# Kernel tuning notes

Measured on AMD Instinct MI355X. Metric: run time of the kernel, lower is better.

The kernel has to match this reference:

```python
import math
import jax, jax.numpy as jnp
import numpy as np

NUM_LAYERS = 4
D_MODEL = 1024
N_HEAD = 8
HEAD_DIM = D_MODEL // N_HEAD
B, L = 8, 512
EPS = 1e-5


def setup_inputs() -> dict:
    key = jax.random.key(0)
    ks = jax.random.split(key, 6)
    x = jax.random.normal(ks[0], (B, L, D_MODEL), dtype=jnp.float32)
    mask = jnp.ones((B, L), dtype=jnp.int32)
    qv_w = jax.random.normal(ks[1], (NUM_LAYERS, 2 * D_MODEL, D_MODEL), dtype=jnp.float32) * 0.02
    r_r_bias = jax.random.normal(ks[2], (NUM_LAYERS, N_HEAD, HEAD_DIM), dtype=jnp.float32) * 0.02
    r_w_bias = jax.random.normal(ks[3], (NUM_LAYERS, N_HEAD, HEAD_DIM), dtype=jnp.float32) * 0.02
    ffn_w = jax.random.normal(ks[4], (NUM_LAYERS, D_MODEL, D_MODEL), dtype=jnp.float32) * 0.02
    ffn_b = jnp.zeros((NUM_LAYERS, D_MODEL), dtype=jnp.float32)
    ln1_g = jnp.ones((NUM_LAYERS, D_MODEL), dtype=jnp.float32)
    ln1_b = jnp.zeros((NUM_LAYERS, D_MODEL), dtype=jnp.float32)
    ln2_g = jnp.ones((NUM_LAYERS, D_MODEL), dtype=jnp.float32)
    ln2_b = jnp.zeros((NUM_LAYERS, D_MODEL), dtype=jnp.float32)
    return dict(x=x, mask=mask, qv_w=qv_w, r_r_bias=r_r_bias, r_w_bias=r_w_bias,
                ln1_g=ln1_g, ln1_b=ln1_b, ffn_w=ffn_w, ffn_b=ffn_b,
                ln2_g=ln2_g, ln2_b=ln2_b)


def _rel_pos_embed(seq_len, dim):
    # weights[p + origin_shift] encodes sinusoid of relative position p;
    # selected positions are arange(-seq_len, seq_len) -> shape [2L, dim]
    half = dim // 2
    inv_freq = jnp.exp(jnp.arange(half, dtype=jnp.float32) * (-math.log(10000.0) / (half - 1)))
    pos = jnp.arange(-seq_len, seq_len, dtype=jnp.float32)
    ang = pos[:, None] * inv_freq[None, :]
    return jnp.concatenate([jnp.sin(ang), jnp.cos(ang)], axis=1)  # [2L, dim]


def _shift(BD):
    # [b,n,L,2L] -> [b,n,L,L] Transformer-XL shift trick
    b, n, l, _ = BD.shape
    BD = jnp.concatenate([BD, jnp.zeros((b, n, l, 1), BD.dtype)], axis=-1)
    BD = BD.reshape(b, n, -1, l)[:, :, :-1].reshape(b, n, l, -1)
    return BD[:, :, :, l:]


def _layernorm(x, g, b):
    mu = jnp.mean(x, axis=-1, keepdims=True)
    var = jnp.mean(jnp.square(x - mu), axis=-1, keepdims=True)
    return (x - mu) * jax.lax.rsqrt(var + EPS) * g + b


def _rel_attn(x, mask, qv_w, rr, rw, pe):
    b, l, d = x.shape
    qv = x @ qv_w.T                      # [b,l,2d]
    q, v = jnp.split(qv, 2, axis=-1)
    q = q.reshape(b, l, N_HEAD, HEAD_DIM).transpose(0, 2, 1, 3)
    k = x.reshape(b, l, N_HEAD, HEAD_DIM).transpose(0, 2, 1, 3)  # raw x as keys (per source)
    v = v.reshape(b, l, N_HEAD, HEAD_DIM).transpose(0, 2, 1, 3)
    AC = jnp.einsum('bnqd,bnkd->bnqk', q + rr[:, None], k)
    D_ = jnp.einsum('nd,ld->nl', rw, pe)[None, :, None]          # [1,n,1,2L]
    B_ = jnp.einsum('bnqd,ld->bnql', q, pe)                      # [b,n,L,2L]
    BD = _shift(B_ + D_)
    attn = AC + BD                                               # scale = 1
    attn = jnp.where(mask[:, None, None, :] == 0, -jnp.inf, attn)
    attn = jax.nn.softmax(attn, axis=-1)
    out = jnp.einsum('bnqk,bnkd->bqnd', attn, v).reshape(b, l, d)
    return out


def reference(x, mask, qv_w, r_r_bias, r_w_bias, ln1_g, ln1_b, ffn_w, ffn_b, ln2_g, ln2_b):
    pe = _rel_pos_embed(x.shape[1], HEAD_DIM)
    h = x
    for i in range(NUM_LAYERS):
        res = h
        h = _rel_attn(h, mask, qv_w[i], r_r_bias[i], r_w_bias[i], pe)
        h = _layernorm(h + res, ln1_g[i], ln1_b[i])
        res = h
        h = jax.nn.relu(h @ ffn_w[i].T + ffn_b[i])
        h = _layernorm(res + h, ln2_g[i], ln2_b[i])
    return h
```

## Files before the change

### kernel.cpp

```cpp
#include <hip/hip_runtime.h>
#include <math.h>

#define NL 4
#define DM 1024
#define NH 8
#define HD 128
#define BB 8
#define LL 512
#define MM (BB*LL)
#define PEN (2*LL)
#define QT 64
#define KT 32
#define NKT (LL/KT)
#define VS 44

typedef __attribute__((ext_vector_type(8))) __bf16 bf16x8;
typedef __attribute__((ext_vector_type(4))) float f32x4;

__device__ __forceinline__ unsigned short f2b(float f) {
  unsigned int u = __float_as_uint(f);
  u = (u + 0x7FFFu + ((u >> 16) & 1u)) >> 16;
  return (unsigned short)u;
}
__device__ __forceinline__ float b2f(unsigned short s) {
  return __uint_as_float(((unsigned int)s) << 16);
}
__device__ __forceinline__ void glds16(const void* g, void* l) {
  __builtin_amdgcn_global_load_lds(
      (const __attribute__((address_space(1))) unsigned int*)g,
      (__attribute__((address_space(3))) unsigned int*)l, 16, 0, 0);
}
union U8 { unsigned short s[8]; bf16x8 v; };
__device__ __forceinline__ void split8(const float4& a, const float4& b,
                                       bf16x8& h, bf16x8& l) {
  float x[8] = {a.x,a.y,a.z,a.w,b.x,b.y,b.z,b.w};
  U8 uh, ul;
#pragma unroll
  for (int e = 0; e < 8; ++e) {
    unsigned u = __float_as_uint(x[e]);
    uh.s[e] = (unsigned short)(u >> 16);
    ul.s[e] = f2b(x[e] - __uint_as_float(u & 0xffff0000u));
  }
  h = uh.v; l = ul.v;
}

__global__ __launch_bounds__(256) void pe_kernel(unsigned short* __restrict__ peh,
                                                 unsigned short* __restrict__ pel) {
  int idx = blockIdx.x * 256 + threadIdx.x;
  if (idx >= PEN * HD) return;
  int p = idx / HD, j = idx % HD;
  int tt = (j < 64) ? j : (j - 64);
  float invf = expf((float)tt * (-9.210340371976184f / 63.0f));
  float ang = (float)(p - LL) * invf;
  float v = (j < 64) ? sinf(ang) : cosf(ang);
  unsigned short h = f2b(v);
  peh[idx] = h;
  pel[idx] = f2b(v - b2f(h));
}

__global__ __launch_bounds__(256) void d2_kernel(const float* __restrict__ rrb,
                                                 const float* __restrict__ rwb,
                                                 const unsigned short* __restrict__ peh,
                                                 const unsigned short* __restrict__ pel,
                                                 float* __restrict__ d2) {
  int idx = blockIdx.x * 256 + threadIdx.x;
  if (idx >= NH * PEN) return;
  int n = idx / PEN, p = idx % PEN;
  float s = 0.f;
  for (int d = 0; d < HD; ++d) {
    float pv = b2f(peh[p*HD + d]) + b2f(pel[p*HD + d]);
    s += (rwb[n*HD + d] - rrb[n*HD + d]) * pv;
  }
  d2[idx] = s;
}

__global__ __launch_bounds__(256) void split_kernel(const float* __restrict__ in,
                                                    unsigned short* __restrict__ hi,
                                                    unsigned short* __restrict__ lo,
                                                    int n) {
  int i = (blockIdx.x * 256 + threadIdx.x) * 4;
  if (i >= n) return;
  float4 v = *(const float4*)&in[i];
  float x[4] = {v.x, v.y, v.z, v.w};
  ushort4 h4, l4;
  unsigned short* hp = (unsigned short*)&h4;
  unsigned short* lp = (unsigned short*)&l4;
#pragma unroll
  for (int e = 0; e < 4; ++e) {
    unsigned short h = f2b(x[e]);
    hp[e] = h;
    lp[e] = f2b(x[e] - b2f(h));
  }
  *(ushort4*)&hi[i] = h4;
  *(ushort4*)&lo[i] = l4;
}

template<bool FFN>
__global__ __launch_bounds__(256) void gemm_mfma(
    const unsigned short* __restrict__ Ah, const unsigned short* __restrict__ Al,
    const float* __restrict__ Bw, const float* __restrict__ bias,
    float* __restrict__ C, unsigned short* __restrict__ Vhi,
    unsigned short* __restrict__ Vlo, int N, int K, int ldc) {
  __shared__ __align__(16) unsigned short AsH[128*64];
  __shared__ __align__(16) unsigned short AsL[128*64];
  __shared__ __align__(16) unsigned short BsH[128*72];
  __shared__ __align__(16) unsigned short BsL[128*72];
  const int t = threadIdx.x;
  const int w = t >> 6, l = t & 63;
  const int gx = gridDim.x;
  const int nwg = gx * gridDim.y;
  const int id = blockIdx.y * gx + blockIdx.x;
  const int swz = (id & 7) * (nwg >> 3) + (id >> 3);
  const int bm = (swz / gx) * 128, bn = (swz % gx) * 128;
  const int wr = (w >> 1) * 64, wc = (w & 1) * 64;

  const int aseg = ((t & 7) ^ ((t >> 3) & 7)) * 8;
  const unsigned short* Ahb = Ah + (size_t)(bm + (t >> 3)) * K + aseg;
  const unsigned short* Alb = Al + (size_t)(bm + (t >> 3)) * K + aseg;

  const int brow = t >> 1, bhalf = (t & 1) * 32;
  const float* Bb = Bw + (size_t)(bn + brow) * K + bhalf;

  f32x4 acc[4][4] = {};
  const int lm = l & 15;
  const int lg = l >> 4;

  for (int k0 = 0; k0 < K; k0 += 64) {
    float4 bv[8];
#pragma unroll
    for (int c = 0; c < 8; ++c)
      bv[c] = *(const float4*)(Bb + k0 + c*4);
#pragma unroll
    for (int i = 0; i < 4; ++i) {
      glds16(Ahb + (size_t)(i*32)*K + k0, &AsH[w*512 + i*2048]);
      glds16(Alb + (size_t)(i*32)*K + k0, &AsL[w*512 + i*2048]);
    }
#pragma unroll
    for (int c = 0; c < 8; ++c) {
      float xs[4] = {bv[c].x, bv[c].y, bv[c].z, bv[c].w};
      ushort4 h4, l4;
      unsigned short* hp = (unsigned short*)&h4;
      unsigned short* lp = (unsigned short*)&l4;
#pragma unroll
      for (int e = 0; e < 4; ++e) {
        unsigned u = __float_as_uint(xs[e]);
        hp[e] = (unsigned short)(u >> 16);
        float r = xs[e] - __uint_as_float(u & 0xffff0000u);
        lp[e] = (unsigned short)(__float_as_uint(r) >> 16);
      }
      *(ushort4*)&BsH[brow*72 + bhalf + c*4] = h4;
      *(ushort4*)&BsL[brow*72 + bhalf + c*4] = l4;
    }
    __syncthreads();

#pragma unroll
    for (int kk = 0; kk < 2; ++kk) {
      bf16x8 afh[4], afl[4], bfh[4], bfl[4];
#pragma unroll
      for (int i = 0; i < 4; ++i) {
        const int row = wr + i*16 + lm;
        const int sw = ((kk*4 + lg) ^ (lm & 7)) * 8;
        afh[i] = *(const bf16x8*)&AsH[row*64 + sw];
        afl[i] = *(const bf16x8*)&AsL[row*64 + sw];
      }
#pragma unroll
      for (int j = 0; j < 4; ++j) {
        bfh[j] = *(const bf16x8*)&BsH[(wc + j*16 + lm)*72 + kk*32 + lg*8];
        bfl[j] = *(const bf16x8*)&BsL[(wc + j*16 + lm)*72 + kk*32 + lg*8];
      }
#pragma unroll
      for (int i = 0; i < 4; ++i)
#pragma unroll
        for (int j = 0; j < 4; ++j) {
          acc[i][j] = __builtin_amdgcn_mfma_f32_16x16x32_bf16(afh[i], bfh[j], acc[i][j], 0, 0, 0);
          acc[i][j] = __builtin_amdgcn_mfma_f32_16x16x32_bf16(afh[i], bfl[j], acc[i][j], 0, 0, 0);
          acc[i][j] = __builtin_amdgcn_mfma_f32_16x16x32_bf16(afl[i], bfh[j], acc[i][j], 0, 0, 0);
        }
    }
    __syncthreads();
  }

  const int cr = (l >> 4) * 4;
  const bool vhalf = (!FFN) && (bn >= DM);
#pragma unroll
  for (int i = 0; i < 4; ++i) {
#pragma unroll
    for (int j = 0; j < 4; ++j) {
      int row = bm + wr + i*16 + cr;
      int col = bn + wc + j*16 + lm;
      float bvl = FFN ? bias[col] : 0.f;
      f32x4 a = acc[i][j];
#pragma unroll
      for (int r4 = 0; r4 < 4; ++r4) {
        float v = a[r4];
        if (FFN) {
          v = fmaxf(v + bvl, 0.f);
          C[(size_t)(row + r4) * ldc + col] = v;
        } else if (vhalf) {
          unsigned u = __float_as_uint(v);
          size_t off = (size_t)(row + r4) * DM + (col - DM);
          Vhi[off] = (unsigned short)(u >> 16);
          Vlo[off] = f2b(v - __uint_as_float(u & 0xffff0000u));
        } else {
          C[(size_t)(row + r4) * ldc + col] = v;
        }
      }
    }
  }
}

__global__ __launch_bounds__(256, 2) void attn_mfma(
    const float* __restrict__ qbuf,
    const unsigned short* __restrict__ khp,
    const unsigned short* __restrict__ klp,
    const unsigned short* __restrict__ vhp,
    const unsigned short* __restrict__ vlp,
    const unsigned short* __restrict__ pehp,
    const unsigned short* __restrict__ pelp,
    const float* __restrict__ rrb,
    const int*   __restrict__ mask,
    const float* __restrict__ d2p,
    float* __restrict__ outp)
{
  __shared__ __align__(16) unsigned short KsH[KT*136];
  __shared__ __align__(16) unsigned short KsL[KT*136];
  __shared__ __align__(16) unsigned short VtH[HD*VS];
  __shared__ __align__(16) unsigned short VtL[HD*VS];
  __shared__ __align__(16) unsigned short PsH[4][16*40];
  __shared__ __align__(16) unsigned short PsL[4][16*40];

  const int id = blockIdx.x + 8*blockIdx.y + 64*blockIdx.z;
  const int n  = id & 7;
  const int qt = (id >> 3) & 7;
  const int b  = id >> 6;
  const int q0 = qt * QT;
  const int t  = threadIdx.x;
  const int w  = t >> 6, l = t & 63;
  const int lm = l & 15, lg = l >> 4;
  const int q0w = q0 + w*16;
  const int r8 = t >> 3, s8 = t & 7;
  const int vr0 = t >> 5, vd4 = (t & 31)*4;

  bf16x8 qah[4], qal[4];
  {
    size_t qrow = (size_t)(b*LL + q0w + lm) * DM + (size_t)n*HD;
#pragma unroll
    for (int c = 0; c < 4; ++c) {
      int d0 = c*32 + lg*8;
      float4 x1 = *(const float4*)&qbuf[qrow + d0];
      float4 x2 = *(const float4*)&qbuf[qrow + d0 + 4];
      float4 r1 = *(const float4*)&rrb[n*HD + d0];
      float4 r2 = *(const float4*)&rrb[n*HD + d0 + 4];
      float4 a = {x1.x+r1.x, x1.y+r1.y, x1.z+r1.z, x1.w+r1.w};
      float4 bq = {x2.x+r2.x, x2.y+r2.y, x2.z+r2.z, x2.w+r2.w};
      split8(a, bq, qah[c], qal[c]);
    }
  }

  {
    size_t krow = (size_t)(b*LL + r8)*DM + (size_t)n*HD + s8*16;
    *(uint4*)&KsH[r8*136 + s8*16]     = *(const uint4*)&khp[krow];
    *(uint4*)&KsH[r8*136 + s8*16 + 8] = *(const uint4*)&khp[krow + 8];
    *(uint4*)&KsL[r8*136 + s8*16]     = *(const uint4*)&klp[krow];
    *(uint4*)&KsL[r8*136 + s8*16 + 8] = *(const uint4*)&klp[krow + 8];
    ushort4 vh[4], vl[4];
#pragma unroll
    for (int i = 0; i < 4; ++i) {
      size_t vrow = (size_t)(b*LL + vr0*4 + i)*DM + n*HD + vd4;
      vh[i] = *(const ushort4*)&vhp[vrow];
      vl[i] = *(const ushort4*)&vlp[vrow];
    }
#pragma unroll
    for (int e = 0; e < 4; ++e) {
      ushort4 th = { ((const unsigned short*)&vh[0])[e], ((const unsigned short*)&vh[1])[e],
                     ((const unsigned short*)&vh[2])[e], ((const unsigned short*)&vh[3])[e] };
      ushort4 tl = { ((const unsigned short*)&vl[0])[e], ((const unsigned short*)&vl[1])[e],
                     ((const unsigned short*)&vl[2])[e], ((const unsigned short*)&vl[3])[e] };
      *(ushort4*)&VtH[(vd4+e)*VS + vr0*4] = th;
      *(ushort4*)&VtL[(vd4+e)*VS + vr0*4] = tl;
    }
  }
  __syncthreads();

  float m_run[4] = {-3.0e38f, -3.0e38f, -3.0e38f, -3.0e38f};
  float l_run[4] = {0.f, 0.f, 0.f, 0.f};
  f32x4 accO[8] = {};
  f32x4 accB0 = {}, accB1 = {}, accB2 = {};

  for (int kt = 0; kt < NKT; ++kt) {
    const int k0 = kt * KT;
    const int base_w = k0 - q0w + 497;

    uint4 kxh0, kxh1, kxl0, kxl1;
    ushort4 vxh[4], vxl[4];
    const bool pf = kt < NKT-1;
    if (pf) {
      size_t krow = (size_t)(b*LL + k0 + KT + r8)*DM + (size_t)n*HD + s8*16;
      kxh0 = *(const uint4*)&khp[krow];     kxh1 = *(const uint4*)&khp[krow + 8];
      kxl0 = *(const uint4*)&klp[krow];     kxl1 = *(const uint4*)&klp[krow + 8];
#pragma unroll
      for (int i = 0; i < 4; ++i) {
        size_t vrow = (size_t)(b*LL + k0 + KT + vr0*4 + i)*DM + n*HD + vd4;
        vxh[i] = *(const ushort4*)&vhp[vrow];
        vxl[i] = *(const ushort4*)&vlp[vrow];
      }
    }

    float d2v1, d2v2;
    {
      int di1 = base_w + 16 + lm; di1 = di1 > PEN-1 ? PEN-1 : di1;
      int di2 = base_w + 32 + lm; di2 = di2 > PEN-1 ? PEN-1 : di2;
      d2v1 = d2p[n*PEN + di1];
      d2v2 = d2p[n*PEN + di2];
    }
    const int msk0 = mask[b*LL + k0 + lm];
    const int msk1 = mask[b*LL + k0 + 16 + lm];

    bf16x8 p1h[4], p1l[4], p2h[4], p2l[4];
    {
      int pr1 = base_w + 16 + lm; pr1 = pr1 > PEN-1 ? PEN-1 : pr1;
      int pr2 = base_w + 32 + lm; pr2 = pr2 > PEN-1 ? PEN-1 : pr2;
      const unsigned short* pb1 = pehp + (size_t)pr1*HD + lg*8;
      const unsigned short* pq1 = pelp + (size_t)pr1*HD + lg*8;
      const unsigned short* pb2 = pehp + (size_t)pr2*HD + lg*8;
      const unsigned short* pq2 = pelp + (size_t)pr2*HD + lg*8;
#pragma unroll
      for (int c = 0; c < 4; ++c) {
        p1h[c] = *(const bf16x8*)(pb1 + c*32);
        p1l[c] = *(const bf16x8*)(pq1 + c*32);
        p2h[c] = *(const bf16x8*)(pb2 + c*32);
        p2l[c] = *(const bf16x8*)(pq2 + c*32);
      }
    }

    __builtin_amdgcn_s_setprio(1);
    f32x4 accA[2] = {};
#pragma unroll
    for (int tt = 0; tt < 2; ++tt)
#pragma unroll
      for (int c = 0; c < 4; ++c) {
        const int krow = tt*16 + lm;
        bf16x8 kfh = *(const bf16x8*)&KsH[krow*136 + (c*4+lg)*8];
        bf16x8 kfl = *(const bf16x8*)&KsL[krow*136 + (c*4+lg)*8];
        accA[tt] = __builtin_amdgcn_mfma_f32_16x16x32_bf16(qah[c], kfh, accA[tt], 0, 0, 0);
        accA[tt] = __builtin_amdgcn_mfma_f32_16x16x32_bf16(qah[c], kfl, accA[tt], 0, 0, 0);
        accA[tt] = __builtin_amdgcn_mfma_f32_16x16x32_bf16(qal[c], kfh, accA[tt], 0, 0, 0);
      }

    if (kt == 0) {
      int pr0 = base_w + lm; pr0 = pr0 > PEN-1 ? PEN-1 : pr0;
      const unsigned short* pb0 = pehp + (size_t)pr0*HD + lg*8;
      const unsigned short* pq0 = pelp + (size_t)pr0*HD + lg*8;
      f32x4 a = {};
#pragma unroll
      for (int c = 0; c < 4; ++c) {
        bf16x8 ph = *(const bf16x8*)(pb0 + c*32);
        bf16x8 pl = *(const bf16x8*)(pq0 + c*32);
        a = __builtin_amdgcn_mfma_f32_16x16x32_bf16(qah[c], ph, a, 0, 0, 0);
        a = __builtin_amdgcn_mfma_f32_16x16x32_bf16(qah[c], pl, a, 0, 0, 0);
        a = __builtin_amdgcn_mfma_f32_16x16x32_bf16(qal[c], ph, a, 0, 0, 0);
      }
      float dv0 = d2p[n*PEN + pr0];
#pragma unroll
      for (int r = 0; r < 4; ++r) a[r] += dv0;
      accB0 = a;
    } else {
      accB0 = accB2;
    }
    {
      f32x4 a = {};
#pragma unroll
      for (int c = 0; c < 4; ++c) {
        a = __builtin_amdgcn_mfma_f32_16x16x32_bf16(qah[c], p1h[c], a, 0, 0, 0);
        a = __builtin_amdgcn_mfma_f32_16x16x32_bf16(qah[c], p1l[c], a, 0, 0, 0);
        a = __builtin_amdgcn_mfma_f32_16x16x32_bf16(qal[c], p1h[c], a, 0, 0, 0);
      }
#pragma unroll
      for (int r = 0; r < 4; ++r) a[r] += d2v1;
      accB1 = a;
    }
    {
      f32x4 a = {};
#pragma unroll
      for (int c = 0; c < 4; ++c) {
        a = __builtin_amdgcn_mfma_f32_16x16x32_bf16(qah[c], p2h[c], a, 0, 0, 0);
        a = __builtin_amdgcn_mfma_f32_16x16x32_bf16(qah[c], p2l[c], a, 0, 0, 0);
        a = __builtin_amdgcn_mfma_f32_16x16x32_bf16(qal[c], p2h[c], a, 0, 0, 0);
      }
#pragma unroll
      for (int r = 0; r < 4; ++r) a[r] += d2v2;
      accB2 = a;
    }
    __builtin_amdgcn_s_setprio(0);

    float s[2][4];
#pragma unroll
    for (int r = 0; r < 4; ++r) {
      const int qi = lg*4 + r;
      const int jm = (lm - qi + 15) & 15;
      const int src = (l & 48) | jm;
      const bool carry = lm > qi;
      float sh0 = __shfl(accB0[r], src);
      float sh1 = __shfl(accB1[r], src);
      float sh2 = __shfl(accB2[r], src);
      float bd0 = carry ? sh1 : sh0;
      float bd1 = carry ? sh2 : sh1;
      float v0 = accA[0][r] + bd0;
      float v1 = accA[1][r] + bd1;
      s[0][r] = (msk0 == 0) ? -1e30f : v0;
      s[1][r] = (msk1 == 0) ? -1e30f : v1;
    }

    float mt4[4];
    int allold = 1;
#pragma unroll
    for (int r = 0; r < 4; ++r) {
      float mt = fmaxf(s[0][r], s[1][r]);
      mt = fmaxf(mt, __shfl_xor(mt, 1));
      mt = fmaxf(mt, __shfl_xor(mt, 2));
      mt = fmaxf(mt, __shfl_xor(mt, 4));
      mt = fmaxf(mt, __shfl_xor(mt, 8));
      mt4[r] = mt;
      allold &= (mt <= m_run[r]) ? 1 : 0;
    }
    if (!__all(allold)) {
#pragma unroll
      for (int r = 0; r < 4; ++r) {
        float mn = fmaxf(m_run[r], mt4[r]);
        float sc = __expf(m_run[r] - mn);
        m_run[r] = mn;
        l_run[r] *= sc;
#pragma unroll
        for (int j8 = 0; j8 < 8; ++j8) accO[j8][r] *= sc;
      }
    }
#pragma unroll
    for (int r = 0; r < 4; ++r) {
      float p0 = __expf(s[0][r] - m_run[r]);
      float p1 = __expf(s[1][r] - m_run[r]);
      s[0][r] = p0; s[1][r] = p1;
      float la = p0 + p1;
      la += __shfl_xor(la, 1);
      la += __shfl_xor(la, 2);
      la += __shfl_xor(la, 4);
      la += __shfl_xor(la, 8);
      l_run[r] += la;
    }

#pragma unroll
    for (int tt = 0; tt < 2; ++tt)
#pragma unroll
      for (int r = 0; r < 4; ++r) {
        int qi = lg*4 + r, kc = tt*16 + lm;
        float p = s[tt][r];
        unsigned u = __float_as_uint(p);
        PsH[w][qi*40 + kc] = (unsigned short)(u >> 16);
        PsL[w][qi*40 + kc] = f2b(p - __uint_as_float(u & 0xffff0000u));
      }

    {
      __builtin_amdgcn_s_setprio(1);
      bf16x8 pah = *(const bf16x8*)&PsH[w][lm*40 + lg*8];
      bf16x8 pal = *(const bf16x8*)&PsL[w][lm*40 + lg*8];
#pragma unroll
      for (int j8 = 0; j8 < 8; ++j8) {
        const int dim = j8*16 + lm;
        bf16x8 vfh = *(const bf16x8*)&VtH[dim*VS + lg*8];
        bf16x8 vfl = *(const bf16x8*)&VtL[dim*VS + lg*8];
        accO[j8] = __builtin_amdgcn_mfma_f32_16x16x32_bf16(pah, vfh, accO[j8], 0, 0, 0);
        accO[j8] = __builtin_amdgcn_mfma_f32_16x16x32_bf16(pah, vfl, accO[j8], 0, 0, 0);
        accO[j8] = __builtin_amdgcn_mfma_f32_16x16x32_bf16(pal, vfh, accO[j8], 0, 0, 0);
      }
      __builtin_amdgcn_s_setprio(0);
    }

    __syncthreads();

    if (pf) {
      *(uint4*)&KsH[r8*136 + s8*16]     = kxh0;
      *(uint4*)&KsH[r8*136 + s8*16 + 8] = kxh1;
      *(uint4*)&KsL[r8*136 + s8*16]     = kxl0;
      *(uint4*)&KsL[r8*136 + s8*16 + 8] = kxl1;
#pragma unroll
      for (int e = 0; e < 4; ++e) {
        ushort4 th = { ((const unsigned short*)&vxh[0])[e], ((const unsigned short*)&vxh[1])[e],
                       ((const unsigned short*)&vxh[2])[e], ((const unsigned short*)&vxh[3])[e] };
        ushort4 tl = { ((const unsigned short*)&vxl[0])[e], ((const unsigned short*)&vxl[1])[e],
                       ((const unsigned short*)&vxl[2])[e], ((const unsigned short*)&vxl[3])[e] };
        *(ushort4*)&VtH[(vd4+e)*VS + vr0*4] = th;
        *(ushort4*)&VtL[(vd4+e)*VS + vr0*4] = tl;
      }
    }
    __syncthreads();
  }

  float inv[4];
#pragma unroll
  for (int r = 0; r < 4; ++r) inv[r] = 1.0f / l_run[r];
#pragma unroll
  for (int j8 = 0; j8 < 8; ++j8)
#pragma unroll
    for (int r = 0; r < 4; ++r)
      outp[(size_t)(b*LL + q0w + lg*4 + r)*DM + n*HD + j8*16 + lm] = accO[j8][r] * inv[r];
}

__global__ __launch_bounds__(256) void add_ln_kernel(
    const float* __restrict__ y, int ys,
    const float* __restrict__ res,
    const float* __restrict__ g, const float* __restrict__ bt,
    float* __restrict__ out,
    unsigned short* __restrict__ ohi, unsigned short* __restrict__ olo)
{
  const int r = blockIdx.x, t = threadIdx.x;
  float4 v = *(const float4*)&y[(size_t)r*ys + t*4];
  float4 w = *(const float4*)&res[(size_t)r*DM + t*4];
  float4 s = {v.x+w.x, v.y+w.y, v.z+w.z, v.w+w.w};
  float sum = s.x + s.y + s.z + s.w;
  float ssq = s.x*s.x + s.y*s.y + s.z*s.z + s.w*s.w;
#pragma unroll
  for (int off = 32; off >= 1; off >>= 1) {
    sum += __shfl_down(sum, off);
    ssq += __shfl_down(ssq, off);
  }
  __shared__ float red[8];
  int wid = t >> 6;
  if ((t & 63) == 0) { red[wid] = sum; red[wid+4] = ssq; }
  __syncthreads();
  float totS = red[0] + red[1] + red[2] + red[3];
  float totQ = red[4] + red[5] + red[6] + red[7];
  float mu  = totS * (1.0f/DM);
  float var = totQ * (1.0f/DM) - mu*mu;
  float inv = rsqrtf(var + 1e-5f);
  float4 gg = *(const float4*)&g[t*4];
  float4 bb = *(const float4*)&bt[t*4];
  float4 o;
  o.x = (s.x - mu)*inv*gg.x + bb.x;
  o.y = (s.y - mu)*inv*gg.y + bb.y;
  o.z = (s.z - mu)*inv*gg.z + bb.z;
  o.w = (s.w - mu)*inv*gg.w + bb.w;
  *(float4*)&out[(size_t)r*DM + t*4] = o;
  float xs[4] = {o.x, o.y, o.z, o.w};
  ushort4 h4, l4;
  unsigned short* hp = (unsigned short*)&h4;
  unsigned short* lp = (unsigned short*)&l4;
#pragma unroll
  for (int e = 0; e < 4; ++e) {
    unsigned short h = f2b(xs[e]);
    hp[e] = h;
    lp[e] = f2b(xs[e] - b2f(h));
  }
  *(ushort4*)&ohi[(size_t)r*DM + t*4] = h4;
  *(ushort4*)&olo[(size_t)r*DM + t*4] = l4;
}

extern "C" void kernel_launch(void* const* d_in, const int* in_sizes, int n_in,
                              void* d_out, int out_size, void* d_ws, size_t ws_size,
                              hipStream_t stream) {
  const float* x    = (const float*)d_in[0];
  const int*   mask = (const int*)d_in[1];
  const float* qv_w = (const float*)d_in[2];
  const float* rrb  = (const float*)d_in[3];
  const float* rwb  = (const float*)d_in[4];
  const float* ln1g = (const float*)d_in[5];
  const float* ln1b = (const float*)d_in[6];
  const float* ffnw = (const float*)d_in[7];
  const float* ffnb = (const float*)d_in[8];
  const float* ln2g = (const float*)d_in[9];
  const float* ln2b = (const float*)d_in[10];

  float* h  = (float*)d_out;
  unsigned short* peh = (unsigned short*)d_ws;
  unsigned short* pel = peh + (size_t)PEN*HD;
  float* d2   = (float*)(pel + (size_t)PEN*HD);
  float* qbuf = d2 + (size_t)NH*PEN;
  unsigned short* vhi = (unsigned short*)(qbuf + (size_t)MM*DM);
  unsigned short* vlo = vhi + (size_t)MM*DM;
  unsigned short* hhi = vlo + (size_t)MM*DM;
  unsigned short* hlo = hhi + (size_t)MM*DM;

  hipMemcpyAsync(h, x, (size_t)MM*DM*sizeof(float), hipMemcpyDeviceToDevice, stream);
  split_kernel<<<(MM*DM)/1024, 256, 0, stream>>>(x, hhi, hlo, MM*DM);
  pe_kernel<<<(PEN*HD)/256, 256, 0, stream>>>(peh, pel);

  for (int l = 0; l < NL; ++l) {
    const float* rr_l = rrb + (size_t)l*NH*HD;
    const float* rw_l = rwb + (size_t)l*NH*HD;
    d2_kernel<<<(NH*PEN)/256, 256, 0, stream>>>(rr_l, rw_l, peh, pel, d2);
    gemm_mfma<false><<<dim3((2*DM)/128, MM/128), 256, 0, stream>>>(
        hhi, hlo, qv_w + (size_t)l*2*DM*DM, nullptr, qbuf, vhi, vlo, 2*DM, DM, DM);
    attn_mfma<<<dim3(LL/QT, NH, BB), 256, 0, stream>>>(
        qbuf, hhi, hlo, vhi, vlo, peh, pel, rr_l, mask, d2, qbuf);
    add_ln_kernel<<<MM, 256, 0, stream>>>(qbuf, DM, h,
        ln1g + (size_t)l*DM, ln1b + (size_t)l*DM, h, hhi, hlo);
    gemm_mfma<true><<<dim3(DM/128, MM/128), 256, 0, stream>>>(
        hhi, hlo, ffnw + (size_t)l*DM*DM, ffnb + (size_t)l*DM, qbuf, nullptr, nullptr, DM, DM, DM);
    add_ln_kernel<<<MM, 256, 0, stream>>>(qbuf, DM, h,
        ln2g + (size_t)l*DM, ln2b + (size_t)l*DM, h, hhi, hlo);
  }
  (void)in_sizes; (void)n_in; (void)out_size; (void)ws_size;
}
```

Measured before the change: 914.9 us.

## Halve attention query tile, drop K-low LDS staging, read K-low fragments from global

The attention kernel now uses 32-query tiles with 128 threads (2 waves) instead of 64 queries with 256 threads, doubling the grid and reordering block indices so heads vary fastest. The low-part bf16 K tile is no longer staged in shared memory. Each wave loads its K-low fragments straight from global and issues those MFMAs after the positional-term work. This cuts LDS footprint and per-block staging, but raises global traffic for K-low and V reloads per query tile. The kt==0 positional index is now also clamped at zero.

```diff
diff --git a/kernel.cpp b/kernel.cpp
--- a/kernel.cpp
+++ b/kernel.cpp
@@ -9,7 +9,7 @@
 #define LL 512
 #define MM (BB*LL)
 #define PEN (2*LL)
-#define QT 64
+#define QT 32
 #define KT 32
 #define NKT (LL/KT)
 #define VS 44
@@ -209,7 +209,7 @@
   }
 }
 
-__global__ __launch_bounds__(256, 2) void attn_mfma(
+__global__ __launch_bounds__(128, 2) void attn_mfma(
     const float* __restrict__ qbuf,
     const unsigned short* __restrict__ khp,
     const unsigned short* __restrict__ klp,
@@ -223,23 +223,21 @@
     float* __restrict__ outp)
 {
   __shared__ __align__(16) unsigned short KsH[KT*136];
-  __shared__ __align__(16) unsigned short KsL[KT*136];
   __shared__ __align__(16) unsigned short VtH[HD*VS];
   __shared__ __align__(16) unsigned short VtL[HD*VS];
-  __shared__ __align__(16) unsigned short PsH[4][16*40];
-  __shared__ __align__(16) unsigned short PsL[4][16*40];
-
-  const int id = blockIdx.x + 8*blockIdx.y + 64*blockIdx.z;
-  const int n  = id & 7;
-  const int qt = (id >> 3) & 7;
-  const int b  = id >> 6;
+  __shared__ __align__(16) unsigned short PsH[2][16*40];
+  __shared__ __align__(16) unsigned short PsL[2][16*40];
+
+  const int n  = blockIdx.x;
+  const int qt = blockIdx.y;
+  const int b  = blockIdx.z;
   const int q0 = qt * QT;
   const int t  = threadIdx.x;
   const int w  = t >> 6, l = t & 63;
   const int lm = l & 15, lg = l >> 4;
   const int q0w = q0 + w*16;
-  const int r8 = t >> 3, s8 = t & 7;
-  const int vr0 = t >> 5, vd4 = (t & 31)*4;
+  const int kr  = t >> 2, ks = (t & 3) * 32;
+  const int vr0 = (t >> 5) * 8, vd4 = (t & 31)*4;
 
   bf16x8 qah[4], qal[4];
   {
@@ -258,26 +256,31 @@
   }
 
   {
-    size_t krow = (size_t)(b*LL + r8)*DM + (size_t)n*HD + s8*16;
-    *(uint4*)&KsH[r8*136 + s8*16]     = *(const uint4*)&khp[krow];
-    *(uint4*)&KsH[r8*136 + s8*16 + 8] = *(const uint4*)&khp[krow + 8];
-    *(uint4*)&KsL[r8*136 + s8*16]     = *(const uint4*)&klp[krow];
-    *(uint4*)&KsL[r8*136 + s8*16 + 8] = *(const uint4*)&klp[krow + 8];
-    ushort4 vh[4], vl[4];
-#pragma unroll
-    for (int i = 0; i < 4; ++i) {
-      size_t vrow = (size_t)(b*LL + vr0*4 + i)*DM + n*HD + vd4;
+    size_t krow = (size_t)(b*LL + kr)*DM + (size_t)n*HD + ks;
+#pragma unroll
+    for (int i = 0; i < 4; ++i)
+      *(uint4*)&KsH[kr*136 + ks + i*8] = *(const uint4*)&khp[krow + i*8];
+    ushort4 vh[8], vl[8];
+#pragma unroll
+    for (int i = 0; i < 8; ++i) {
+      size_t vrow = (size_t)(b*LL + vr0 + i)*DM + n*HD + vd4;
       vh[i] = *(const ushort4*)&vhp[vrow];
       vl[i] = *(const ushort4*)&vlp[vrow];
     }
 #pragma unroll
     for (int e = 0; e < 4; ++e) {
-      ushort4 th = { ((const unsigned short*)&vh[0])[e], ((const unsigned short*)&vh[1])[e],
+      ushort4 ta = { ((const unsigned short*)&vh[0])[e], ((const unsigned short*)&vh[1])[e],
                      ((const unsigned short*)&vh[2])[e], ((const unsigned short*)&vh[3])[e] };
-      ushort4 tl = { ((const unsigned short*)&vl[0])[e], ((const unsigned short*)&vl[1])[e],
+      ushort4 tb = { ((const unsigned short*)&vh[4])[e], ((const unsigned short*)&vh[5])[e],
+                     ((const unsigned short*)&vh[6])[e], ((const unsigned short*)&vh[7])[e] };
+      ushort4 tc = { ((const unsigned short*)&vl[0])[e], ((const unsigned short*)&vl[1])[e],
                      ((const unsigned short*)&vl[2])[e], ((const unsigned short*)&vl[3])[e] };
-      *(ushort4*)&VtH[(vd4+e)*VS + vr0*4] = th;
-      *(ushort4*)&VtL[(vd4+e)*VS + vr0*4] = tl;
+      ushort4 td = { ((const unsigned short*)&vl[4])[e], ((const unsigned short*)&vl[5])[e],
+                     ((const unsigned short*)&vl[6])[e], ((const unsigned short*)&vl[7])[e] };
+      *(ushort4*)&VtH[(vd4+e)*VS + vr0]     = ta;
+      *(ushort4*)&VtH[(vd4+e)*VS + vr0 + 4] = tb;
+      *(ushort4*)&VtL[(vd4+e)*VS + vr0]     = tc;
+      *(ushort4*)&VtL[(vd4+e)*VS + vr0 + 4] = td;
     }
   }
   __syncthreads();
@@ -291,16 +294,17 @@
     const int k0 = kt * KT;
     const int base_w = k0 - q0w + 497;
 
-    uint4 kxh0, kxh1, kxl0, kxl1;
-    ushort4 vxh[4], vxl[4];
+    uint4 kxh[4];
+    ushort4 vxh[8], vxl[8];
     const bool pf = kt < NKT-1;
     if (pf) {
-      size_t krow = (size_t)(b*LL + k0 + KT + r8)*DM + (size_t)n*HD + s8*16;
-      kxh0 = *(const uint4*)&khp[krow];     kxh1 = *(const uint4*)&khp[krow + 8];
-      kxl0 = *(const uint4*)&klp[krow];     kxl1 = *(const uint4*)&klp[krow + 8];
-#pragma unroll
-      for (int i = 0; i < 4; ++i) {
-        size_t vrow = (size_t)(b*LL + k0 + KT + vr0*4 + i)*DM + n*HD + vd4;
+      size_t krow = (size_t)(b*LL + k0 + KT + kr)*DM + (size_t)n*HD + ks;
+#pragma unroll
+      for (int i = 0; i < 4; ++i)
+        kxh[i] = *(const uint4*)&khp[krow + i*8];
+#pragma unroll
+      for (int i = 0; i < 8; ++i) {
+        size_t vrow = (size_t)(b*LL + k0 + KT + vr0 + i)*DM + n*HD + vd4;
         vxh[i] = *(const ushort4*)&vhp[vrow];
         vxl[i] = *(const ushort4*)&vlp[vrow];
       }
@@ -315,6 +319,13 @@
     }
     const int msk0 = mask[b*LL + k0 + lm];
     const int msk1 = mask[b*LL + k0 + 16 + lm];
+
+    bf16x8 klo_f[2][4];
+#pragma unroll
+    for (int tt = 0; tt < 2; ++tt)
+#pragma unroll
+      for (int c = 0; c < 4; ++c)
+        klo_f[tt][c] = *(const bf16x8*)&klp[(size_t)(b*LL + k0 + tt*16 + lm)*DM + n*HD + c*32 + lg*8];
 
     bf16x8 p1h[4], p1l[4], p2h[4], p2l[4];
     {
@@ -339,16 +350,14 @@
     for (int tt = 0; tt < 2; ++tt)
 #pragma unroll
       for (int c = 0; c < 4; ++c) {
-        const int krow = tt*16 + lm;
-        bf16x8 kfh = *(const bf16x8*)&KsH[krow*136 + (c*4+lg)*8];
-        bf16x8 kfl = *(const bf16x8*)&KsL[krow*136 + (c*4+lg)*8];
+        const int krw = tt*16 + lm;
+        bf16x8 kfh = *(const bf16x8*)&KsH[krw*136 + (c*4+lg)*8];
         accA[tt] = __builtin_amdgcn_mfma_f32_16x16x32_bf16(qah[c], kfh, accA[tt], 0, 0, 0);
-        accA[tt] = __builtin_amdgcn_mfma_f32_16x16x32_bf16(qah[c], kfl, accA[tt], 0, 0, 0);
         accA[tt] = __builtin_amdgcn_mfma_f32_16x16x32_bf16(qal[c], kfh, accA[tt], 0, 0, 0);
       }
 
     if (kt == 0) {
-      int pr0 = base_w + lm; pr0 = pr0 > PEN-1 ? PEN-1 : pr0;
+      int pr0 = base_w + lm; pr0 = pr0 < 0 ? 0 : (pr0 > PEN-1 ? PEN-1 : pr0);
       const unsigned short* pb0 = pehp + (size_t)pr0*HD + lg*8;
       const unsigned short* pq0 = pelp + (size_t)pr0*HD + lg*8;
       f32x4 a = {};
@@ -391,6 +400,12 @@
       for (int r = 0; r < 4; ++r) a[r] += d2v2;
       accB2 = a;
     }
+
+#pragma unroll
+    for (int tt = 0; tt < 2; ++tt)
+#pragma unroll
+      for (int c = 0; c < 4; ++c)
+        accA[tt] = __builtin_amdgcn_mfma_f32_16x16x32_bf16(qah[c], klo_f[tt][c], accA[tt], 0, 0, 0);
     __builtin_amdgcn_s_setprio(0);
 
     float s[2][4];
@@ -477,18 +492,23 @@
     __syncthreads();
 
     if (pf) {
-      *(uint4*)&KsH[r8*136 + s8*16]     = kxh0;
-      *(uint4*)&KsH[r8*136 + s8*16 + 8] = kxh1;
-      *(uint4*)&KsL[r8*136 + s8*16]     = kxl0;
-      *(uint4*)&KsL[r8*136 + s8*16 + 8] = kxl1;
+#pragma unroll
+      for (int i = 0; i < 4; ++i)
+        *(uint4*)&KsH[kr*136 + ks + i*8] = kxh[i];
 #pragma unroll
       for (int e = 0; e < 4; ++e) {
-        ushort4 th = { ((const unsigned short*)&vxh[0])[e], ((const unsigned short*)&vxh[1])[e],
+        ushort4 ta = { ((const unsigned short*)&vxh[0])[e], ((const unsigned short*)&vxh[1])[e],
                        ((const unsigned short*)&vxh[2])[e], ((const unsigned short*)&vxh[3])[e] };
-        ushort4 tl = { ((const unsigned short*)&vxl[0])[e], ((const unsigned short*)&vxl[1])[e],
+        ushort4 tb = { ((const unsigned short*)&vxh[4])[e], ((const unsigned short*)&vxh[5])[e],
+                       ((const unsigned short*)&vxh[6])[e], ((const unsigned short*)&vxh[7])[e] };
+        ushort4 tc = { ((const unsigned short*)&vxl[0])[e], ((const unsigned short*)&vxl[1])[e],
                        ((const unsigned short*)&vxl[2])[e], ((const unsigned short*)&vxl[3])[e] };
-        *(ushort4*)&VtH[(vd4+e)*VS + vr0*4] = th;
-        *(ushort4*)&VtL[(vd4+e)*VS + vr0*4] = tl;
+        ushort4 td = { ((const unsigned short*)&vxl[4])[e], ((const unsigned short*)&vxl[5])[e],
+                       ((const unsigned short*)&vxl[6])[e], ((const unsigned short*)&vxl[7])[e] };
+        *(ushort4*)&VtH[(vd4+e)*VS + vr0]     = ta;
+        *(ushort4*)&VtH[(vd4+e)*VS + vr0 + 4] = tb;
+        *(ushort4*)&VtL[(vd4+e)*VS + vr0]     = tc;
+        *(ushort4*)&VtL[(vd4+e)*VS + vr0 + 4] = td;
       }
     }
     __syncthreads();
@@ -588,7 +608,7 @@
     d2_kernel<<<(NH*PEN)/256, 256, 0, stream>>>(rr_l, rw_l, peh, pel, d2);
     gemm_mfma<false><<<dim3((2*DM)/128, MM/128), 256, 0, stream>>>(
         hhi, hlo, qv_w + (size_t)l*2*DM*DM, nullptr, qbuf, vhi, vlo, 2*DM, DM, DM);
-    attn_mfma<<<dim3(LL/QT, NH, BB), 256, 0, stream>>>(
+    attn_mfma<<<dim3(NH, LL/QT, BB), 128, 0, stream>>>(
         qbuf, hhi, hlo, vhi, vlo, peh, pel, rr_l, mask, d2, qbuf);
     add_ln_kernel<<<MM, 256, 0, stream>>>(qbuf, DM, h,
         ln1g + (size_t)l*DM, ln1b + (size_t)l*DM, h, hhi, hlo);
```

Result: slower. 1.140 ms (+24.6%).
